# Performance work log

Measured on AMD Instinct MI355X. Metric: run time of the kernel, lower is better.

Reference implementation:

```python
import jax, jax.numpy as jnp
import numpy as np

C = 128
IC = C // 2  # inter_channels
EPS = 1e-5   # InstanceNorm2d default eps (affine=False -> no learned scale/shift)


def setup_inputs() -> dict:
    key = jax.random.key(0)
    ks = jax.random.split(key, 9)
    s = 0.05
    return {
        "x": jax.random.normal(ks[0], (4, C, 64, 64), dtype=jnp.float32),
        "g_w": jax.random.normal(ks[1], (IC, C), dtype=jnp.float32) * s,
        "g_b": jax.random.normal(ks[2], (IC,), dtype=jnp.float32) * s,
        "theta_w": jax.random.normal(ks[3], (IC, C), dtype=jnp.float32) * s,
        "theta_b": jax.random.normal(ks[4], (IC,), dtype=jnp.float32) * s,
        "phi_w": jax.random.normal(ks[5], (IC, C), dtype=jnp.float32) * s,
        "phi_b": jax.random.normal(ks[6], (IC,), dtype=jnp.float32) * s,
        "W_w": jax.random.normal(ks[7], (C, IC), dtype=jnp.float32) * s,
        "W_b": jax.random.normal(ks[8], (C,), dtype=jnp.float32) * s,
    }


def reference(x, g_w, g_b, theta_w, theta_b, phi_w, phi_b, W_w, W_b):
    B, Cc, H, Wd = x.shape
    N = H * Wd
    xf = x.reshape(B, Cc, N)  # [B, C, N]

    def proj(w, b):  # 1x1 conv == channel matmul
        return jnp.einsum('oc,bcn->bon', w, xf) + b[:, None]  # [B, IC, N]

    g_x = proj(g_w, g_b).transpose(0, 2, 1)        # [B, N, IC]
    theta_x = proj(theta_w, theta_b).transpose(0, 2, 1)  # [B, N, IC]
    phi_x = proj(phi_w, phi_b)                     # [B, IC, N]

    f = jnp.einsum('bnc,bcm->bnm', theta_x, phi_x)  # [B, N, N] unscaled affinity
    f = jax.nn.softmax(f, axis=-1)
    y = jnp.einsum('bnm,bmc->bnc', f, g_x)          # [B, N, IC]
    y = y.transpose(0, 2, 1)                        # [B, IC, N]

    W_y = jnp.einsum('oc,bcn->bon', W_w, y) + W_b[:, None]  # [B, C, N]
    # InstanceNorm2d (affine=False): normalize per (batch, channel) over spatial
    mean = W_y.mean(axis=-1, keepdims=True)
    var = W_y.var(axis=-1, keepdims=True)
    W_y = (W_y - mean) * jax.lax.rsqrt(var + EPS)

    return x + W_y.reshape(B, Cc, H, Wd)
```

## Files before the change

kernel.cpp:

```cpp
#include <hip/hip_runtime.h>
#include <math.h>

typedef __attribute__((ext_vector_type(4))) float f32x4;
typedef __attribute__((ext_vector_type(8))) short s16x8;
typedef __attribute__((ext_vector_type(4))) unsigned int u32x4;
typedef __attribute__((ext_vector_type(2))) unsigned int u32x2;

#define NB 4
#define CH 128
#define ICH 64
#define NSP 4096
#define KSPLIT 8
#define SEGK (NSP / KSPLIT)
#define LDK 72

static __device__ __forceinline__ unsigned short f2bf(float f) {
  unsigned int u = __builtin_bit_cast(unsigned int, f);
  u += 0x7fffu + ((u >> 16) & 1u);
  return (unsigned short)(u >> 16);
}

__global__ __launch_bounds__(256) void k_wconv(
    const float* __restrict__ tw, const float* __restrict__ pw,
    const float* __restrict__ gw, const float* __restrict__ Ww,
    unsigned short* __restrict__ Wwb, float* __restrict__ stat)
{
  int i = blockIdx.x * 256 + threadIdx.x;
  int which = i >> 11;
  const float* src = (which == 0) ? tw : (which == 1) ? pw : (which == 2) ? gw : Ww;
  float4 v = ((const float4*)src)[i & 2047];
  unsigned int p0 = (unsigned int)f2bf(v.x) | ((unsigned int)f2bf(v.y) << 16);
  unsigned int p1 = (unsigned int)f2bf(v.z) | ((unsigned int)f2bf(v.w) << 16);
  *(u32x2*)(Wwb + i * 4) = (u32x2){p0, p1};
  if (blockIdx.x == 0) {
    float4 z = {0.f, 0.f, 0.f, 0.f};
    ((float4*)stat)[threadIdx.x] = z;
  }
}

__global__ __launch_bounds__(128) void k_proj(
    const float* __restrict__ x,
    const float* __restrict__ gbias, const float* __restrict__ tbias,
    const float* __restrict__ pbias,
    const unsigned short* __restrict__ Wwb,
    unsigned short* __restrict__ thetaT, unsigned short* __restrict__ phiT,
    unsigned short* __restrict__ gout)
{
  __shared__ __align__(16) unsigned short ldsT[32 * LDK];
  const int b = blockIdx.y;
  const int n0 = blockIdx.x * 32;
  const int t = threadIdx.x;
  const int wave = t >> 6, lane = t & 63;
  const int l15 = lane & 15, quad = lane >> 4;
  const int n = n0 + wave * 16 + l15;
  const float* xb = x + (size_t)b * CH * NSP;

  s16x8 aq[4];
#pragma unroll
  for (int kc = 0; kc < 4; ++kc)
#pragma unroll
    for (int j = 0; j < 8; ++j)
      aq[kc][j] = (short)f2bf(xb[(size_t)(kc * 32 + quad * 8 + j) * NSP + n]);

  unsigned short* myT = &ldsT[wave * 16 * LDK];
  const int erow = lane >> 3, ecol = (lane & 7) * 8;

#pragma unroll
  for (int z = 0; z < 3; ++z) {
    const float* Bz = (z == 0) ? tbias : (z == 1) ? pbias : gbias;
    const float scl = (z == 0) ? 1.44269504f : 1.0f;
    const unsigned short* Wz = Wwb + z * (ICH * CH);
#pragma unroll
    for (int osub = 0; osub < 4; ++osub) {
      f32x4 acc = (f32x4){0.f, 0.f, 0.f, 0.f};
#pragma unroll
      for (int kc = 0; kc < 4; ++kc) {
        s16x8 bw = __builtin_bit_cast(s16x8,
            *(const u32x4*)(Wz + (osub * 16 + l15) * CH + kc * 32 + quad * 8));
        acc = __builtin_amdgcn_mfma_f32_16x16x32_bf16(aq[kc], bw, acc, 0, 0, 0);
      }
      float bv = Bz[osub * 16 + l15];
#pragma unroll
      for (int r = 0; r < 4; ++r)
        myT[(quad * 4 + r) * LDK + osub * 16 + l15] = f2bf((acc[r] + bv) * scl);
    }
    if (z < 2) {
      unsigned short* outp = ((z == 0) ? thetaT : phiT) + ((size_t)b * NSP + n0 + wave * 16) * ICH;
      u32x4 w0 = *(const u32x4*)(&myT[erow * LDK + ecol]);
      u32x4 w1 = *(const u32x4*)(&myT[(8 + erow) * LDK + ecol]);
      *(u32x4*)(outp + erow * ICH + ecol) = w0;
      *(u32x4*)(outp + (8 + erow) * ICH + ecol) = w1;
    } else {
      __syncthreads();
#pragma unroll
      for (int jj = 0; jj < 2; ++jj) {
        int o = (wave * 2 + jj) * 16 + (lane >> 2);
        int nch = (lane & 3) * 8;
        unsigned short vv[8];
#pragma unroll
        for (int q2 = 0; q2 < 8; ++q2) vv[q2] = ldsT[(nch + q2) * LDK + o];
        unsigned int words[4];
#pragma unroll
        for (int i2 = 0; i2 < 4; ++i2)
          words[i2] = (unsigned int)vv[2 * i2] | ((unsigned int)vv[2 * i2 + 1] << 16);
        *(u32x4*)(gout + ((size_t)b * ICH + o) * NSP + n0 + nch) =
            (u32x4){words[0], words[1], words[2], words[3]};
      }
    }
  }
}

__global__ __launch_bounds__(256, 2) void k_attn(
    const unsigned short* __restrict__ thetaT,
    const unsigned short* __restrict__ phiT,
    const unsigned short* __restrict__ gmat,
    unsigned short* __restrict__ Opart, float* __restrict__ lpart)
{
  __shared__ unsigned short ldsK[64 * LDK];
  __shared__ unsigned short ldsV[64 * LDK];
  __shared__ unsigned short ldsP[4][16 * LDK];
  const int qt = blockIdx.x, b = blockIdx.y, seg = blockIdx.z;
  const int t = threadIdx.x;
  const int wave = t >> 6, lane = t & 63;
  const int l15 = lane & 15, quad = lane >> 4;
  const int q0 = qt * 256 + wave * 64;

  s16x8 aq[4][2];
  const unsigned short* th = thetaT + ((size_t)b * NSP + q0) * ICH;
#pragma unroll
  for (int qs = 0; qs < 4; ++qs)
#pragma unroll
    for (int ks = 0; ks < 2; ++ks)
      aq[qs][ks] = __builtin_bit_cast(s16x8,
          *(const u32x4*)(th + (qs * 16 + l15) * ICH + ks * 32 + quad * 8));

  f32x4 Oacc[4][4];
  f32x4 lacc[4];
#pragma unroll
  for (int i = 0; i < 4; ++i) {
    lacc[i] = (f32x4){0.f, 0.f, 0.f, 0.f};
#pragma unroll
    for (int j = 0; j < 4; ++j) Oacc[i][j] = (f32x4){0.f, 0.f, 0.f, 0.f};
  }

  s16x8 bones;
  {
    short v = (l15 == 0) ? (short)0x3F80 : (short)0;
#pragma unroll
    for (int j = 0; j < 8; ++j) bones[j] = v;
  }

  const unsigned short* ph = phiT + (size_t)b * NSP * ICH;
  const unsigned short* gb = gmat + (size_t)b * ICH * NSP;
  const int k0 = seg * SEGK;

  for (int kt = 0; kt < SEGK / 64; ++kt) {
    const int key0 = k0 + kt * 64;
    __syncthreads();
#pragma unroll
    for (int i = 0; i < 4; ++i) {
      int idx = t + 256 * i;
      int rr = (idx >> 3) & 63, c8 = (idx & 7) * 8;
      if (idx < 512)
        *(u32x4*)(&ldsK[rr * LDK + c8]) =
            *(const u32x4*)(ph + (size_t)(key0 + rr) * ICH + c8);
      else
        *(u32x4*)(&ldsV[rr * LDK + c8]) =
            *(const u32x4*)(gb + (size_t)rr * NSP + key0 + c8);
    }
    __syncthreads();

    s16x8 bk[4][2];
#pragma unroll
    for (int kc = 0; kc < 4; ++kc)
#pragma unroll
      for (int ks = 0; ks < 2; ++ks)
        bk[kc][ks] = *(const s16x8*)(&ldsK[(kc * 16 + l15) * LDK + ks * 32 + quad * 8]);
    s16x8 bv[2][4];
#pragma unroll
    for (int ks = 0; ks < 2; ++ks)
#pragma unroll
      for (int ds = 0; ds < 4; ++ds)
        bv[ks][ds] = *(const s16x8*)(&ldsV[(ds * 16 + l15) * LDK + ks * 32 + quad * 8]);

    unsigned short* myP = &ldsP[wave][0];
#pragma unroll
    for (int qs = 0; qs < 4; ++qs) {
#pragma unroll
      for (int kc = 0; kc < 4; ++kc) {
        f32x4 sacc = (f32x4){0.f, 0.f, 0.f, 0.f};
        sacc = __builtin_amdgcn_mfma_f32_16x16x32_bf16(aq[qs][0], bk[kc][0], sacc, 0, 0, 0);
        sacc = __builtin_amdgcn_mfma_f32_16x16x32_bf16(aq[qs][1], bk[kc][1], sacc, 0, 0, 0);
#pragma unroll
        for (int r = 0; r < 4; ++r) {
          float e = exp2f(sacc[r]);
          myP[(quad * 4 + r) * LDK + kc * 16 + l15] =
              (unsigned short)(__builtin_bit_cast(unsigned int, e) >> 16);
        }
      }
#pragma unroll
      for (int ks = 0; ks < 2; ++ks) {
        s16x8 ap = *(const s16x8*)(&myP[l15 * LDK + ks * 32 + quad * 8]);
        lacc[qs] = __builtin_amdgcn_mfma_f32_16x16x32_bf16(ap, bones, lacc[qs], 0, 0, 0);
#pragma unroll
        for (int ds = 0; ds < 4; ++ds)
          Oacc[qs][ds] = __builtin_amdgcn_mfma_f32_16x16x32_bf16(ap, bv[ks][ds], Oacc[qs][ds], 0, 0, 0);
      }
    }
  }

  unsigned short* Ob = Opart + (((size_t)seg * NB + b) * NSP + q0) * ICH;
  unsigned short* myP = &ldsP[wave][0];
  const int erow = lane >> 3;
  const int ecol = (lane & 7) * 8;
#pragma unroll
  for (int qs = 0; qs < 4; ++qs) {
#pragma unroll
    for (int ds = 0; ds < 4; ++ds)
#pragma unroll
      for (int r = 0; r < 4; ++r)
        myP[(quad * 4 + r) * LDK + ds * 16 + l15] = f2bf(Oacc[qs][ds][r]);
    u32x4 w0 = *(const u32x4*)(&myP[erow * LDK + ecol]);
    u32x4 w1 = *(const u32x4*)(&myP[(8 + erow) * LDK + ecol]);
    *(u32x4*)(Ob + (qs * 16 + erow) * ICH + ecol) = w0;
    *(u32x4*)(Ob + (qs * 16 + 8 + erow) * ICH + ecol) = w1;
  }
  {
    float* myPf = (float*)myP;
    if (l15 == 0) {
#pragma unroll
      for (int qs = 0; qs < 4; ++qs)
#pragma unroll
        for (int r = 0; r < 4; ++r)
          myPf[qs * 16 + quad * 4 + r] = lacc[qs][r];
    }
    float* lb = lpart + ((size_t)seg * NB + b) * NSP + q0;
    lb[lane] = myPf[lane];
  }
}

__global__ __launch_bounds__(128) void k_wy(
    const unsigned short* __restrict__ Opart, const float* __restrict__ lpart,
    const unsigned short* __restrict__ Wwb,
    float* __restrict__ WyT, float* __restrict__ stat)
{
  const int b = blockIdx.y, nt = blockIdx.x;
  const int t = threadIdx.x;
  const int wave = t >> 6, lane = t & 63;
  const int l15 = lane & 15, quad = lane >> 4;
  const int n0 = nt * 32 + wave * 16;
  float ls = 0.f;
#pragma unroll
  for (int s = 0; s < KSPLIT; ++s)
    ls += lpart[((size_t)s * NB + b) * NSP + n0 + l15];
  float inv = 1.0f / ls;
  s16x8 ay[2];
#pragma unroll
  for (int ks = 0; ks < 2; ++ks) {
    float acc8[8];
#pragma unroll
    for (int j = 0; j < 8; ++j) acc8[j] = 0.f;
#pragma unroll
    for (int s = 0; s < KSPLIT; ++s) {
      const unsigned short* op =
          Opart + (((size_t)s * NB + b) * NSP + n0 + l15) * ICH + ks * 32 + quad * 8;
      u32x4 raw = *(const u32x4*)op;
#pragma unroll
      for (int w2 = 0; w2 < 4; ++w2) {
        unsigned int u = raw[w2];
        acc8[2 * w2]     += __builtin_bit_cast(float, u << 16);
        acc8[2 * w2 + 1] += __builtin_bit_cast(float, u & 0xFFFF0000u);
      }
    }
#pragma unroll
    for (int j = 0; j < 8; ++j) ay[ks][j] = (short)f2bf(acc8[j] * inv);
  }
  const unsigned short* Wb = Wwb + 3 * (ICH * CH);
  s16x8 bw[8][2];
#pragma unroll
  for (int cc = 0; cc < 8; ++cc)
#pragma unroll
    for (int ks = 0; ks < 2; ++ks)
      bw[cc][ks] = __builtin_bit_cast(s16x8,
          *(const u32x4*)(Wb + (cc * 16 + l15) * ICH + ks * 32 + quad * 8));
  float sums[8], sq[8];
#pragma unroll
  for (int cc = 0; cc < 8; ++cc) { sums[cc] = 0.f; sq[cc] = 0.f; }
#pragma unroll
  for (int cc = 0; cc < 8; ++cc) {
    f32x4 acc = (f32x4){0.f, 0.f, 0.f, 0.f};
    acc = __builtin_amdgcn_mfma_f32_16x16x32_bf16(ay[0], bw[cc][0], acc, 0, 0, 0);
    acc = __builtin_amdgcn_mfma_f32_16x16x32_bf16(ay[1], bw[cc][1], acc, 0, 0, 0);
    float* wout = WyT + ((size_t)b * NSP + n0 + quad * 4) * CH + cc * 16 + l15;
#pragma unroll
    for (int r = 0; r < 4; ++r) {
      float v = acc[r];
      sums[cc] += v;
      sq[cc] += v * v;
      wout[r * CH] = v;
    }
  }
#pragma unroll
  for (int cc = 0; cc < 8; ++cc) {
    sums[cc] += __shfl_xor(sums[cc], 16, 64);
    sums[cc] += __shfl_xor(sums[cc], 32, 64);
    sq[cc] += __shfl_xor(sq[cc], 16, 64);
    sq[cc] += __shfl_xor(sq[cc], 32, 64);
  }
  if (quad == 0) {
#pragma unroll
    for (int cc = 0; cc < 8; ++cc) {
      atomicAdd(&stat[(b * CH + cc * 16 + l15) * 2 + 0], sums[cc]);
      atomicAdd(&stat[(b * CH + cc * 16 + l15) * 2 + 1], sq[cc]);
    }
  }
}

__global__ __launch_bounds__(256) void k_norm(
    const float* __restrict__ WyT, const float* __restrict__ stat,
    const float* __restrict__ x, float* __restrict__ out)
{
  __shared__ float sWy[32 * 132];
  const int nt = blockIdx.x;
  const int b = blockIdx.y;
  const int t = threadIdx.x;
  const int n0 = nt * 32;
#pragma unroll
  for (int i = 0; i < 4; ++i) {
    int idx = t + 256 * i;
    int row = idx >> 5, c4 = idx & 31;
    *(float4*)(&sWy[row * 132 + c4 * 4]) =
        *(const float4*)(WyT + ((size_t)b * NSP + n0 + row) * CH + c4 * 4);
  }
  __syncthreads();
#pragma unroll
  for (int j = 0; j < 4; ++j) {
    int u = t + 256 * j;
    int co = u >> 3, nq = u & 7;
    float s = stat[(b * CH + co) * 2 + 0];
    float ss = stat[(b * CH + co) * 2 + 1];
    float mean = s * (1.f / NSP);
    float var = ss * (1.f / NSP) - mean * mean;
    float rs = rsqrtf(var + 1e-5f);
    float4 xv = *(const float4*)(x + (size_t)(b * CH + co) * NSP + n0 + nq * 4);
    float4 ov;
    ov.x = xv.x + (sWy[(nq * 4 + 0) * 132 + co] - mean) * rs;
    ov.y = xv.y + (sWy[(nq * 4 + 1) * 132 + co] - mean) * rs;
    ov.z = xv.z + (sWy[(nq * 4 + 2) * 132 + co] - mean) * rs;
    ov.w = xv.w + (sWy[(nq * 4 + 3) * 132 + co] - mean) * rs;
    *(float4*)(out + (size_t)(b * CH + co) * NSP + n0 + nq * 4) = ov;
  }
}

extern "C" void kernel_launch(void* const* d_in, const int* in_sizes, int n_in,
                              void* d_out, int out_size, void* d_ws, size_t ws_size,
                              hipStream_t stream)
{
  const float* x  = (const float*)d_in[0];
  const float* gw = (const float*)d_in[1];
  const float* gb = (const float*)d_in[2];
  const float* tw = (const float*)d_in[3];
  const float* tb = (const float*)d_in[4];
  const float* pw = (const float*)d_in[5];
  const float* pb = (const float*)d_in[6];
  const float* Ww = (const float*)d_in[7];
  float* out = (float*)d_out;
  char* ws = (char*)d_ws;
  unsigned short* thetaT = (unsigned short*)(ws);
  unsigned short* phiT   = (unsigned short*)(ws + (2ull << 20));
  unsigned short* gmat   = (unsigned short*)(ws + (4ull << 20));
  float* WyT   = (float*)(ws + (8ull << 20));
  float* stat  = (float*)(ws + (16ull << 20));
  unsigned short* Wwb = (unsigned short*)(ws + (16ull << 20) + 65536);
  float* lpart = (float*)(ws + (16ull << 20) + (1ull << 19));
  unsigned short* Opart = (unsigned short*)(ws + (17ull << 20));

  k_wconv<<<dim3(32), 256, 0, stream>>>(tw, pw, gw, Ww, Wwb, stat);
  k_proj<<<dim3(128, 4), 128, 0, stream>>>(x, gb, tb, pb, Wwb, thetaT, phiT, gmat);
  k_attn<<<dim3(16, 4, KSPLIT), 256, 0, stream>>>(thetaT, phiT, gmat, Opart, lpart);
  k_wy<<<dim3(128, 4), 128, 0, stream>>>(Opart, lpart, Wwb, WyT, stat);
  k_norm<<<dim3(128, 4), 256, 0, stream>>>(WyT, stat, x, out);
}
```

Before: 142.2 us.

## Double-buffer K/V tiles in attention kernel with register prefetch

The attention kernel now loads the next K/V tile from global memory into registers before computing on the current tile, then writes it to the alternate LDS buffer after compute. This drops one barrier per iteration and is meant to hide global-load latency behind the MFMA work. In exchange it doubles the K/V LDS footprint and adds prefetch registers, which may lower occupancy under the 2-blocks-per-CU launch bound.

```diff
diff --git a/kernel.cpp b/kernel.cpp
--- a/kernel.cpp
+++ b/kernel.cpp
@@ -116,8 +116,8 @@
     const unsigned short* __restrict__ gmat,
     unsigned short* __restrict__ Opart, float* __restrict__ lpart)
 {
-  __shared__ unsigned short ldsK[64 * LDK];
-  __shared__ unsigned short ldsV[64 * LDK];
+  __shared__ unsigned short ldsK[2][64 * LDK];
+  __shared__ unsigned short ldsV[2][64 * LDK];
   __shared__ unsigned short ldsP[4][16 * LDK];
   const int qt = blockIdx.x, b = blockIdx.y, seg = blockIdx.z;
   const int t = threadIdx.x;
@@ -154,34 +154,48 @@
   const unsigned short* gb = gmat + (size_t)b * ICH * NSP;
   const int k0 = seg * SEGK;
 
-  for (int kt = 0; kt < SEGK / 64; ++kt) {
-    const int key0 = k0 + kt * 64;
-    __syncthreads();
+  auto load_tile = [&](int key0, u32x4* pf) {
 #pragma unroll
     for (int i = 0; i < 4; ++i) {
       int idx = t + 256 * i;
-      int rr = (idx >> 3) & 63, c8 = (idx & 7) * 8;
-      if (idx < 512)
-        *(u32x4*)(&ldsK[rr * LDK + c8]) =
-            *(const u32x4*)(ph + (size_t)(key0 + rr) * ICH + c8);
-      else
-        *(u32x4*)(&ldsV[rr * LDK + c8]) =
-            *(const u32x4*)(gb + (size_t)rr * NSP + key0 + c8);
-    }
-    __syncthreads();
+      int r2 = (idx >> 3) & 63, c8 = (idx & 7) * 8;
+      pf[i] = (idx < 512)
+          ? *(const u32x4*)(ph + (size_t)(key0 + r2) * ICH + c8)
+          : *(const u32x4*)(gb + (size_t)r2 * NSP + key0 + c8);
+    }
+  };
+  auto store_tile = [&](int buf, const u32x4* pf) {
+#pragma unroll
+    for (int i = 0; i < 4; ++i) {
+      int idx = t + 256 * i;
+      int r2 = (idx >> 3) & 63, c8 = (idx & 7) * 8;
+      if (idx < 512) *(u32x4*)(&ldsK[buf][r2 * LDK + c8]) = pf[i];
+      else           *(u32x4*)(&ldsV[buf][r2 * LDK + c8]) = pf[i];
+    }
+  };
+
+  u32x4 pf[4];
+  load_tile(k0, pf);
+  store_tile(0, pf);
+  __syncthreads();
+
+  for (int kt = 0; kt < SEGK / 64; ++kt) {
+    const int cur = kt & 1;
+    const bool more = (kt + 1) < SEGK / 64;
+    if (more) load_tile(k0 + (kt + 1) * 64, pf);
 
     s16x8 bk[4][2];
 #pragma unroll
     for (int kc = 0; kc < 4; ++kc)
 #pragma unroll
       for (int ks = 0; ks < 2; ++ks)
-        bk[kc][ks] = *(const s16x8*)(&ldsK[(kc * 16 + l15) * LDK + ks * 32 + quad * 8]);
+        bk[kc][ks] = *(const s16x8*)(&ldsK[cur][(kc * 16 + l15) * LDK + ks * 32 + quad * 8]);
     s16x8 bv[2][4];
 #pragma unroll
     for (int ks = 0; ks < 2; ++ks)
 #pragma unroll
       for (int ds = 0; ds < 4; ++ds)
-        bv[ks][ds] = *(const s16x8*)(&ldsV[(ds * 16 + l15) * LDK + ks * 32 + quad * 8]);
+        bv[ks][ds] = *(const s16x8*)(&ldsV[cur][(ds * 16 + l15) * LDK + ks * 32 + quad * 8]);
 
     unsigned short* myP = &ldsP[wave][0];
 #pragma unroll
@@ -206,6 +220,11 @@
         for (int ds = 0; ds < 4; ++ds)
           Oacc[qs][ds] = __builtin_amdgcn_mfma_f32_16x16x32_bf16(ap, bv[ks][ds], Oacc[qs][ds], 0, 0, 0);
       }
+    }
+
+    if (more) {
+      store_tile(cur ^ 1, pf);
+      __syncthreads();
     }
   }
 
```

New measurement: 139.7 us (median of 2 runs). Within noise of the previous version (-1.8%).
